# Kernel optimization log

Hardware: AMD Instinct MI355X
Metric: run time of the kernel (lower is better)

## Reference

```python
import jax, jax.numpy as jnp
import numpy as np

PI_2 = 3.14159 / 2  # matches torch module constant (not exact pi/2, keeps tan finite)
EPS_SUM = 1e-07
EPS_COS = 1e-08  # torch F.cosine_similarity default eps


def setup_inputs() -> dict:
    key = jax.random.key(0)
    k1, k2 = jax.random.split(key)
    B, N, C, H, W = 16, 2000, 512, 7, 7
    # memory is uniform-initialized then sum-normalized per cube, as in __init__
    memory = jax.random.uniform(k1, (N, C, H, W), dtype=jnp.float32)
    memory = memory / (jnp.sum(memory, axis=(1, 2, 3), keepdims=True) + EPS_SUM)
    key_t = jax.random.uniform(k2, (B, C, H, W), dtype=jnp.float32)
    return {"key": key_t, "memory": memory}


def reference(key, memory):
    # _normalize: divide key by its per-sample sum
    k = key / (jnp.sum(key, axis=(1, 2, 3), keepdims=True) + EPS_SUM)
    B = k.shape[0]
    N = memory.shape[0]
    kf = k.reshape(B, -1)            # [B, D], D = C*H*W
    mf = memory.reshape(N, -1)       # [N, D]
    # cosine similarity (torch clamps each norm to eps)
    dots = jnp.einsum('bd,nd->bn', kf, mf)                       # [B, N]
    kn = jnp.maximum(jnp.linalg.norm(kf, axis=-1), EPS_COS)      # [B]
    mn = jnp.maximum(jnp.linalg.norm(mf, axis=-1), EPS_COS)      # [N]
    cos = dots / (kn[:, None] * mn[None, :])
    w = jax.nn.softmax(jnp.tan(cos * PI_2), axis=1)              # [B, N]
    # read: sum over memory cubes weighted by address w
    return jnp.einsum('bn,nchw->bchw', w, memory)                # [B, C, H, W]
```

## Files before the change

kernel.cpp:

```cpp
#include <hip/hip_runtime.h>
#include <math.h>

#define B 16
#define N 2000
#define D 25088
#define D4 6272
#define PI2 1.570795f
#define KC 16
#define KSPAN (D / KC)
#define KTILES (KSPAN / 32)
#define NT (D / 32)
#define NCHUNK 25
#define NPER (N / NCHUNK)
#define SELHI 0x07060302u

typedef __attribute__((ext_vector_type(8))) short short8;
typedef __attribute__((ext_vector_type(4))) float f32x4;
typedef unsigned int uint;

union pk { uint4 u; short8 s; };
__device__ __forceinline__ short8 as_s8(uint4 u) { pk p; p.u = u; return p.s; }

__device__ __forceinline__ float wave_sum(float v) {
#pragma unroll
    for (int off = 32; off > 0; off >>= 1) v += __shfl_xor(v, off, 64);
    return v;
}
__device__ __forceinline__ float wave_max(float v) {
#pragma unroll
    for (int off = 32; off > 0; off >>= 1) v = fmaxf(v, __shfl_xor(v, off, 64));
    return v;
}

__device__ __forceinline__ void cvt_hilo(const float4& a, const float4& b,
                                         short8& hi, short8& lo, float& msq) {
    float xs[8] = {a.x, a.y, a.z, a.w, b.x, b.y, b.z, b.w};
    uint lu[8];
#pragma unroll
    for (int j = 0; j < 8; ++j) {
        uint u = __float_as_uint(xs[j]);
        float lof = xs[j] - __uint_as_float(u & 0xffff0000u);
        lu[j] = __float_as_uint(lof);
        msq = fmaf(xs[j], xs[j], msq);
    }
    uint4 h, l;
    h.x = __builtin_amdgcn_perm(__float_as_uint(xs[1]), __float_as_uint(xs[0]), SELHI);
    h.y = __builtin_amdgcn_perm(__float_as_uint(xs[3]), __float_as_uint(xs[2]), SELHI);
    h.z = __builtin_amdgcn_perm(__float_as_uint(xs[5]), __float_as_uint(xs[4]), SELHI);
    h.w = __builtin_amdgcn_perm(__float_as_uint(xs[7]), __float_as_uint(xs[6]), SELHI);
    l.x = __builtin_amdgcn_perm(lu[1], lu[0], SELHI);
    l.y = __builtin_amdgcn_perm(lu[3], lu[2], SELHI);
    l.z = __builtin_amdgcn_perm(lu[5], lu[4], SELHI);
    l.w = __builtin_amdgcn_perm(lu[7], lu[6], SELHI);
    hi = as_s8(h); lo = as_s8(l);
}

__global__ void k_split(const float* __restrict__ key, unsigned short* __restrict__ ksw,
                        float* __restrict__ kn2) {
    const int tid  = threadIdx.x;
    const int g    = blockIdx.x * 256 + tid;
    const int tile = g >> 6, lane = g & 63;
    const int m = lane & 15, quad = lane >> 4;
    const float* src = key + (size_t)m * D + tile * 32 + quad * 8;
    float4 x0 = *(const float4*)src;
    float4 x1 = *(const float4*)(src + 4);
    short8 hi, lo;
    float ssq = 0.f;
    cvt_hilo(x0, x1, hi, lo, ssq);
    pk ph; ph.s = hi;
    pk pl; pl.s = lo;
    *(uint4*)(ksw + ((size_t)tile * 64 + lane) * 8)        = ph.u;
    *(uint4*)(ksw + ((size_t)(NT + tile) * 64 + lane) * 8) = pl.u;

    ssq += __shfl_xor(ssq, 16, 64);
    ssq += __shfl_xor(ssq, 32, 64);
    __shared__ float lds[4][16];
    if (quad == 0) lds[tid >> 6][m] = ssq;
    __syncthreads();
    if (tid < 16)
        atomicAdd(&kn2[tid], lds[0][tid] + lds[1][tid] + lds[2][tid] + lds[3][tid]);
}

__global__ __launch_bounds__(256, 2) void k_dots(const float* __restrict__ mem,
                                                 const unsigned short* __restrict__ ksw,
                                                 float* __restrict__ dpart,
                                                 float* __restrict__ mpart) {
    const int tid  = threadIdx.x;
    const int lane = tid & 63;
    const int wave = tid >> 6;
    const int n0   = blockIdx.x * 16;
    const int kc   = blockIdx.y * 4 + wave;
    const int nrow = lane & 15, quad = lane >> 4;

    const float4* mrow4 = (const float4*)(mem + (size_t)(n0 + nrow) * D + kc * KSPAN) + quad * 2;
    const uint4* khp = (const uint4*)(ksw + ((size_t)(kc * KTILES) * 64 + lane) * 8);
    const uint4* klp = (const uint4*)(ksw + ((size_t)(NT + kc * KTILES) * 64 + lane) * 8);

    f32x4 ahh = {0.f, 0.f, 0.f, 0.f};
    f32x4 ahl = ahh, alh = ahh;
    float msq = 0.f;

    float4 c0 = mrow4[0], c1 = mrow4[1];
    uint4 kah = khp[0],  kal = klp[0];

    for (int t = 0; t < KTILES; ++t) {
        const int tn = (t + 1 < KTILES) ? t + 1 : t;
        float4 p0 = mrow4[(size_t)tn * 8];
        float4 p1 = mrow4[(size_t)tn * 8 + 1];
        uint4 pah = khp[(size_t)tn * 64];
        uint4 pal = klp[(size_t)tn * 64];

        short8 bh, bl;
        cvt_hilo(c0, c1, bh, bl, msq);
        short8 ah = as_s8(kah), al = as_s8(kal);
        ahh = __builtin_amdgcn_mfma_f32_16x16x32_bf16(ah, bh, ahh, 0, 0, 0);
        ahl = __builtin_amdgcn_mfma_f32_16x16x32_bf16(ah, bl, ahl, 0, 0, 0);
        alh = __builtin_amdgcn_mfma_f32_16x16x32_bf16(al, bh, alh, 0, 0, 0);

        c0 = p0; c1 = p1; kah = pah; kal = pal;
    }

    f32x4 dt;
#pragma unroll
    for (int r = 0; r < 4; ++r) dt[r] = ahh[r] + ahl[r] + alh[r];
#pragma unroll
    for (int r = 0; r < 4; ++r)
        dpart[((size_t)kc * B + quad * 4 + r) * N + n0 + nrow] = dt[r];

    msq += __shfl_xor(msq, 16, 64);
    msq += __shfl_xor(msq, 32, 64);
    if (quad == 0) mpart[(size_t)kc * N + n0 + nrow] = msq;
}

__global__ __launch_bounds__(256, 2) void k_softmax(const float* __restrict__ kn2,
                                                    const float* __restrict__ dpart,
                                                    const float* __restrict__ mpart,
                                                    float* __restrict__ w) {
    const int b = blockIdx.x, tid = threadIdx.x;
    const int wv = tid >> 6, ln = tid & 63;
    __shared__ float t[N];
    __shared__ float redB[4], redC[4];

    const float kn = fmaxf(sqrtf(kn2[b]), 1e-8f);

    float mx = -1e30f;
    for (int n = tid; n < N; n += 256) {
        float ds = 0.f, ms = 0.f;
#pragma unroll
        for (int kc = 0; kc < KC; ++kc) {
            ds += dpart[((size_t)kc * B + b) * N + n];
            ms += mpart[(size_t)kc * N + n];
        }
        float mn = fmaxf(sqrtf(ms), 1e-8f);
        float tv = tanf(ds / (kn * mn) * PI2);
        t[n] = tv;
        mx = fmaxf(mx, tv);
    }
    mx = wave_max(mx);
    if (ln == 0) redB[wv] = mx;
    __syncthreads();
    mx = fmaxf(fmaxf(redB[0], redB[1]), fmaxf(redB[2], redB[3]));

    float sum = 0.f;
    for (int n = tid; n < N; n += 256) {
        float e = expf(t[n] - mx);
        t[n] = e;
        sum += e;
    }
    sum = wave_sum(sum);
    if (ln == 0) redC[wv] = sum;
    __syncthreads();
    sum = redC[0] + redC[1] + redC[2] + redC[3];
    const float inv = 1.f / sum;
    for (int n = tid; n < N; n += 256) w[(size_t)b * N + n] = t[n] * inv;
}

__global__ __launch_bounds__(256, 2) void k_out_p(const float4* __restrict__ mem,
                                                  const float* __restrict__ w,
                                                  float4* __restrict__ part) {
    const int tid = threadIdx.x;
    const int d4  = blockIdx.x * 256 + tid;
    const int n0  = blockIdx.y * NPER;

    __shared__ float wt[B * NPER];
    for (int i = tid; i < B * NPER; i += 256)
        wt[i] = w[(size_t)(i / NPER) * N + n0 + (i % NPER)];
    __syncthreads();
    if (d4 >= D4) return;

    const float4* mp = mem + (size_t)n0 * D4 + d4;
    float4 acc[B];
#pragma unroll
    for (int b = 0; b < B; ++b) acc[b] = make_float4(0.f, 0.f, 0.f, 0.f);

    float4 cur[8];
#pragma unroll
    for (int u = 0; u < 8; ++u) cur[u] = mp[(size_t)u * D4];

#pragma unroll
    for (int g = 0; g < NPER / 8; ++g) {
        const int gn = (g + 1 < NPER / 8) ? g + 1 : g;
        float4 nxt[8];
#pragma unroll
        for (int u = 0; u < 8; ++u) nxt[u] = mp[(size_t)(gn * 8 + u) * D4];
#pragma unroll
        for (int b = 0; b < B; ++b) {
            float4 a = acc[b];
#pragma unroll
            for (int u = 0; u < 8; ++u) {
                const float wv = wt[b * NPER + g * 8 + u];
                a.x = fmaf(wv, cur[u].x, a.x); a.y = fmaf(wv, cur[u].y, a.y);
                a.z = fmaf(wv, cur[u].z, a.z); a.w = fmaf(wv, cur[u].w, a.w);
            }
            acc[b] = a;
        }
#pragma unroll
        for (int u = 0; u < 8; ++u) cur[u] = nxt[u];
    }
#pragma unroll
    for (int b = 0; b < B; ++b)
        part[((size_t)blockIdx.y * B + b) * D4 + d4] = acc[b];
}

__global__ void k_reduce(const float4* __restrict__ part, float4* __restrict__ out) {
    const int i = blockIdx.x * 256 + threadIdx.x;
    float4 s = part[i];
#pragma unroll
    for (int c = 1; c < NCHUNK; ++c) {
        float4 p = part[(size_t)c * B * D4 + i];
        s.x += p.x; s.y += p.y; s.z += p.z; s.w += p.w;
    }
    out[i] = s;
}

__global__ __launch_bounds__(256, 2) void k_out_atomic(const float4* __restrict__ mem,
                                                       const float* __restrict__ w,
                                                       float* __restrict__ out) {
    const int tid = threadIdx.x;
    const int d4  = blockIdx.x * 256 + tid;
    const int n0  = blockIdx.y * NPER;
    __shared__ float wt[B * NPER];
    for (int i = tid; i < B * NPER; i += 256)
        wt[i] = w[(size_t)(i / NPER) * N + n0 + (i % NPER)];
    __syncthreads();
    if (d4 >= D4) return;
    const float4* mp = mem + (size_t)n0 * D4 + d4;
    float4 acc[B];
#pragma unroll
    for (int b = 0; b < B; ++b) acc[b] = make_float4(0.f, 0.f, 0.f, 0.f);
    for (int n = 0; n < NPER; n += 8) {
        float4 mv[8];
#pragma unroll
        for (int u = 0; u < 8; ++u) mv[u] = mp[(size_t)(n + u) * D4];
#pragma unroll
        for (int b = 0; b < B; ++b) {
            float4 a = acc[b];
#pragma unroll
            for (int u = 0; u < 8; ++u) {
                const float wv = wt[b * NPER + n + u];
                a.x = fmaf(wv, mv[u].x, a.x); a.y = fmaf(wv, mv[u].y, a.y);
                a.z = fmaf(wv, mv[u].z, a.z); a.w = fmaf(wv, mv[u].w, a.w);
            }
            acc[b] = a;
        }
    }
#pragma unroll
    for (int b = 0; b < B; ++b) {
        float* op = out + (size_t)b * D + (size_t)d4 * 4;
        unsafeAtomicAdd(op + 0, acc[b].x);
        unsafeAtomicAdd(op + 1, acc[b].y);
        unsafeAtomicAdd(op + 2, acc[b].z);
        unsafeAtomicAdd(op + 3, acc[b].w);
    }
}

extern "C" void kernel_launch(void* const* d_in, const int* in_sizes, int n_in,
                              void* d_out, int out_size, void* d_ws, size_t ws_size,
                              hipStream_t stream) {
    const float* key = (const float*)d_in[0];
    const float* mem = (const float*)d_in[1];
    float* out = (float*)d_out;

    float* ws = (float*)d_ws;
    unsigned short* ksw = (unsigned short*)ws;
    float* dpart = ws + 401408;
    float* mpart = dpart + (size_t)KC * B * N;
    float* kn2   = mpart + (size_t)KC * N;
    float* w     = kn2 + 16;
    float* part  = w + (size_t)B * N;
    const size_t need_full =
        (size_t)(401408 + (size_t)KC * B * N + KC * N + 16 + B * N + (size_t)NCHUNK * B * D) * 4;

    hipMemsetAsync(kn2, 0, 16 * sizeof(float), stream);
    k_split<<<dim3(NT * 64 / 256), 256, 0, stream>>>(key, ksw, kn2);
    k_dots<<<dim3(N / 16, 4), 256, 0, stream>>>(mem, ksw, dpart, mpart);
    k_softmax<<<dim3(B), 256, 0, stream>>>(kn2, dpart, mpart, w);
    if (ws_size >= need_full) {
        k_out_p<<<dim3((D4 + 255) / 256, NCHUNK), 256, 0, stream>>>((const float4*)mem, w, (float4*)part);
        k_reduce<<<dim3(B * D4 / 256), 256, 0, stream>>>((const float4*)part, (float4*)out);
    } else {
        hipMemsetAsync(d_out, 0, (size_t)B * D * sizeof(float), stream);
        k_out_atomic<<<dim3((D4 + 255) / 256, NCHUNK), 256, 0, stream>>>((const float4*)mem, w, out);
    }
}
```

Before: 359.3 us.

## Split dot-product reduction into more K chunks and double-buffer tile loads

Raises the number of K-dimension chunks in the similarity kernel from 16 to 28, so the grid launches more blocks, each with a shorter K loop. The loop is unrolled by two, so loads for the next two tiles are in flight while the current ones feed the MFMA units. The squared-norm accumulator is split into four independent partial sums to shorten the FMA dependency chain. The cost is more partial results for the softmax kernel to sum, a larger workspace, and higher register pressure from the deeper prefetch.

```diff
diff --git a/kernel.cpp b/kernel.cpp
--- a/kernel.cpp
+++ b/kernel.cpp
@@ -6,7 +6,7 @@
 #define D 25088
 #define D4 6272
 #define PI2 1.570795f
-#define KC 16
+#define KC 28
 #define KSPAN (D / KC)
 #define KTILES (KSPAN / 32)
 #define NT (D / 32)
@@ -33,15 +33,16 @@
 }
 
 __device__ __forceinline__ void cvt_hilo(const float4& a, const float4& b,
-                                         short8& hi, short8& lo, float& msq) {
+                                         short8& hi, short8& lo, float4& msqv) {
     float xs[8] = {a.x, a.y, a.z, a.w, b.x, b.y, b.z, b.w};
+    float* mq = &msqv.x;
     uint lu[8];
 #pragma unroll
     for (int j = 0; j < 8; ++j) {
         uint u = __float_as_uint(xs[j]);
         float lof = xs[j] - __uint_as_float(u & 0xffff0000u);
         lu[j] = __float_as_uint(lof);
-        msq = fmaf(xs[j], xs[j], msq);
+        mq[j & 3] = fmaf(xs[j], xs[j], mq[j & 3]);
     }
     uint4 h, l;
     h.x = __builtin_amdgcn_perm(__float_as_uint(xs[1]), __float_as_uint(xs[0]), SELHI);
@@ -65,13 +66,14 @@
     float4 x0 = *(const float4*)src;
     float4 x1 = *(const float4*)(src + 4);
     short8 hi, lo;
-    float ssq = 0.f;
-    cvt_hilo(x0, x1, hi, lo, ssq);
+    float4 msqv = {0.f, 0.f, 0.f, 0.f};
+    cvt_hilo(x0, x1, hi, lo, msqv);
     pk ph; ph.s = hi;
     pk pl; pl.s = lo;
     *(uint4*)(ksw + ((size_t)tile * 64 + lane) * 8)        = ph.u;
     *(uint4*)(ksw + ((size_t)(NT + tile) * 64 + lane) * 8) = pl.u;
 
+    float ssq = (msqv.x + msqv.y) + (msqv.z + msqv.w);
     ssq += __shfl_xor(ssq, 16, 64);
     ssq += __shfl_xor(ssq, 32, 64);
     __shared__ float lds[4][16];
@@ -98,26 +100,38 @@
 
     f32x4 ahh = {0.f, 0.f, 0.f, 0.f};
     f32x4 ahl = ahh, alh = ahh;
-    float msq = 0.f;
-
-    float4 c0 = mrow4[0], c1 = mrow4[1];
-    uint4 kah = khp[0],  kal = klp[0];
-
-    for (int t = 0; t < KTILES; ++t) {
-        const int tn = (t + 1 < KTILES) ? t + 1 : t;
-        float4 p0 = mrow4[(size_t)tn * 8];
-        float4 p1 = mrow4[(size_t)tn * 8 + 1];
-        uint4 pah = khp[(size_t)tn * 64];
-        uint4 pal = klp[(size_t)tn * 64];
+    float4 msqv = {0.f, 0.f, 0.f, 0.f};
+
+    float4 a0 = mrow4[0], a1 = mrow4[1];
+    uint4  ha = khp[0],   la = klp[0];
+    float4 b0 = mrow4[8], b1 = mrow4[9];
+    uint4  hb = khp[64],  lb = klp[64];
+
+    for (int t = 0; t < KTILES; t += 2) {
+        const int t2 = (t + 2 < KTILES) ? t + 2 : t;
+        const int t3 = (t + 3 < KTILES) ? t + 3 : t;
+        float4 na0 = mrow4[(size_t)t2 * 8], na1 = mrow4[(size_t)t2 * 8 + 1];
+        uint4  nha = khp[(size_t)t2 * 64],  nla = klp[(size_t)t2 * 64];
+        float4 nb0 = mrow4[(size_t)t3 * 8], nb1 = mrow4[(size_t)t3 * 8 + 1];
+        uint4  nhb = khp[(size_t)t3 * 64],  nlb = klp[(size_t)t3 * 64];
 
         short8 bh, bl;
-        cvt_hilo(c0, c1, bh, bl, msq);
-        short8 ah = as_s8(kah), al = as_s8(kal);
-        ahh = __builtin_amdgcn_mfma_f32_16x16x32_bf16(ah, bh, ahh, 0, 0, 0);
-        ahl = __builtin_amdgcn_mfma_f32_16x16x32_bf16(ah, bl, ahl, 0, 0, 0);
-        alh = __builtin_amdgcn_mfma_f32_16x16x32_bf16(al, bh, alh, 0, 0, 0);
-
-        c0 = p0; c1 = p1; kah = pah; kal = pal;
+        cvt_hilo(a0, a1, bh, bl, msqv);
+        {
+            short8 kh = as_s8(ha), kl = as_s8(la);
+            ahh = __builtin_amdgcn_mfma_f32_16x16x32_bf16(kh, bh, ahh, 0, 0, 0);
+            ahl = __builtin_amdgcn_mfma_f32_16x16x32_bf16(kh, bl, ahl, 0, 0, 0);
+            alh = __builtin_amdgcn_mfma_f32_16x16x32_bf16(kl, bh, alh, 0, 0, 0);
+        }
+        cvt_hilo(b0, b1, bh, bl, msqv);
+        {
+            short8 kh = as_s8(hb), kl = as_s8(lb);
+            ahh = __builtin_amdgcn_mfma_f32_16x16x32_bf16(kh, bh, ahh, 0, 0, 0);
+            ahl = __builtin_amdgcn_mfma_f32_16x16x32_bf16(kh, bl, ahl, 0, 0, 0);
+            alh = __builtin_amdgcn_mfma_f32_16x16x32_bf16(kl, bh, alh, 0, 0, 0);
+        }
+        a0 = na0; a1 = na1; ha = nha; la = nla;
+        b0 = nb0; b1 = nb1; hb = nhb; lb = nlb;
     }
 
     f32x4 dt;
@@ -127,6 +141,7 @@
     for (int r = 0; r < 4; ++r)
         dpart[((size_t)kc * B + quad * 4 + r) * N + n0 + nrow] = dt[r];
 
+    float msq = (msqv.x + msqv.y) + (msqv.z + msqv.w);
     msq += __shfl_xor(msq, 16, 64);
     msq += __shfl_xor(msq, 32, 64);
     if (quad == 0) mpart[(size_t)kc * N + n0 + nrow] = msq;
@@ -289,11 +304,12 @@
     float* w     = kn2 + 16;
     float* part  = w + (size_t)B * N;
     const size_t need_full =
-        (size_t)(401408 + (size_t)KC * B * N + KC * N + 16 + B * N + (size_t)NCHUNK * B * D) * 4;
+        (size_t)(401408 + (size_t)KC * B * N + (size_t)KC * N + 16 + B * N +
+                 (size_t)NCHUNK * B * D) * 4;
 
     hipMemsetAsync(kn2, 0, 16 * sizeof(float), stream);
     k_split<<<dim3(NT * 64 / 256), 256, 0, stream>>>(key, ksw, kn2);
-    k_dots<<<dim3(N / 16, 4), 256, 0, stream>>>(mem, ksw, dpart, mpart);
+    k_dots<<<dim3(N / 16, KC / 4), 256, 0, stream>>>(mem, ksw, dpart, mpart);
     k_softmax<<<dim3(B), 256, 0, stream>>>(kn2, dpart, mpart, w);
     if (ws_size >= need_full) {
         k_out_p<<<dim3((D4 + 255) / 256, NCHUNK), 256, 0, stream>>>((const float4*)mem, w, (float4*)part);
```

After: 353.8 us. No clear change (-1.5%).
